# Kernel tuning notes

Measured on AMD Instinct MI355X. Metric: run time of the kernel, lower is better.

## Reference

```python
import jax, jax.numpy as jnp
import numpy as np

EPS = 1e-5       # norm_eps
CHUNK = 64       # scan checkpoint chunk size

def _short_conv(x, w):
    # causal depthwise conv (kernel K) + SiLU; x:[B,T,C], w:[C,K]
    K = w.shape[1]
    T = x.shape[1]
    xp = jnp.pad(x, ((0, 0), (K - 1, 0), (0, 0)))
    y = sum(xp[:, i:i + T, :] * w[:, i] for i in range(K))
    return jax.nn.silu(y)

def _l2norm(x):
    return x * jax.lax.rsqrt(jnp.sum(x * x, -1, keepdims=True) + 1e-6)

def _forward(hidden_states, Wq, Wk, Wv, conv_q, conv_k, conv_v, Wf1, Wf2, Wb,
             A_log, dt_bias, Wg, bg, o_norm_w, Wo):
    B, T, _ = hidden_states.shape
    H = A_log.shape[0]
    x = hidden_states
    q = _short_conv(x @ Wq, conv_q)
    k = _short_conv(x @ Wk, conv_k)
    v = _short_conv(x @ Wv, conv_v)
    Dk = q.shape[-1] // H
    Dv = v.shape[-1] // H
    q = _l2norm(q.reshape(B, T, H, Dk))
    k = _l2norm(k.reshape(B, T, H, Dk))
    v = v.reshape(B, T, H, Dv)
    beta = jax.nn.sigmoid(x @ Wb)                               # [B,T,H]
    g = ((x @ Wf1) @ Wf2).reshape(B, T, H, Dk)
    # KDA gate: g = -exp(A_log) * softplus(g + dt_bias), per head & key channel
    g = -jnp.exp(A_log)[:, None] * jax.nn.softplus(g + dt_bias.reshape(H, Dk))
    gexp = jnp.exp(g)                                           # decay in (0,1)
    scale = Dk ** -0.5

    def step(S, inp):
        q_t, k_t, v_t, ge_t, b_t = inp                          # [B,H,Dk]..., [B,H]
        S = S * ge_t[..., None]                                 # per-key-channel decay
        kv = jnp.einsum('bhk,bhkv->bhv', k_t, S)                # current prediction
        upd = (v_t - kv) * b_t[..., None]                       # delta-rule update
        S = S + jnp.einsum('bhk,bhv->bhkv', k_t, upd)
        o_t = jnp.einsum('bhk,bhkv->bhv', q_t, S) * scale
        return S, o_t

    @jax.checkpoint
    def chunk_fn(S, chunk):
        return jax.lax.scan(step, S, chunk)

    def tm(a):  # [B,T,...] -> [T//CHUNK, CHUNK, B, ...]
        a = jnp.moveaxis(a, 1, 0)
        return a.reshape((T // CHUNK, CHUNK) + a.shape[1:])

    S0 = jnp.zeros((B, H, Dk, Dv), dtype=q.dtype)
    _, o = jax.lax.scan(chunk_fn, S0, (tm(q), tm(k), tm(v), tm(gexp), tm(beta)))
    o = jnp.moveaxis(o.reshape((T, B, H, Dv)), 0, 1)            # [B,T,H,Dv]

    gate_o = (x @ Wg + bg).reshape(B, T, H, Dv)
    on = o * jax.lax.rsqrt(jnp.mean(o * o, -1, keepdims=True) + EPS) * o_norm_w
    on = on * jax.nn.silu(gate_o)                               # gated RMSNorm
    return on.reshape(B, T, H * Dv) @ Wo


def setup_inputs() -> dict:
    key = jax.random.key(0)
    ks = jax.random.split(key, 16)
    B, T, D = 2, 2048, 2048
    H, Dk, Dv, K = 16, 128, 128, 4
    n = jax.random.normal
    return {
        'hidden_states': n(ks[0], (B, T, D), jnp.float32),
        'Wq': n(ks[1], (D, H * Dk), jnp.float32) * D ** -0.5,
        'Wk': n(ks[2], (D, H * Dk), jnp.float32) * D ** -0.5,
        'Wv': n(ks[3], (D, H * Dv), jnp.float32) * D ** -0.5,
        'conv_q': n(ks[4], (H * Dk, K), jnp.float32) * 0.5,
        'conv_k': n(ks[5], (H * Dk, K), jnp.float32) * 0.5,
        'conv_v': n(ks[6], (H * Dv, K), jnp.float32) * 0.5,
        'Wf1': n(ks[7], (D, Dv), jnp.float32) * D ** -0.5,
        'Wf2': n(ks[8], (Dv, H * Dk), jnp.float32) * Dv ** -0.5,
        'Wb': n(ks[9], (D, H), jnp.float32) * D ** -0.5,
        'A_log': jnp.log(jax.random.uniform(ks[10], (H,), jnp.float32, 1.0, 16.0)),
        'dt_bias': jnp.zeros((H * Dk,), jnp.float32),
        'Wg': n(ks[11], (D, H * Dv), jnp.float32) * D ** -0.5,
        'bg': jnp.zeros((H * Dv,), jnp.float32),
        'o_norm_w': jnp.ones((Dv,), jnp.float32),
        'Wo': n(ks[12], (H * Dv, D), jnp.float32) * (H * Dv) ** -0.5,
    }


def reference(hidden_states, Wq, Wk, Wv, conv_q, conv_k, conv_v, Wf1, Wf2, Wb,
              A_log, dt_bias, Wg, bg, o_norm_w, Wo):
    return _forward(hidden_states, Wq, Wk, Wv, conv_q, conv_k, conv_v, Wf1, Wf2,
                    Wb, A_log, dt_bias, Wg, bg, o_norm_w, Wo)
```

## Files before the change

### kernel.cpp

```cpp
#include <hip/hip_runtime.h>
#include <stdint.h>

#define BB 2
#define TT 2048
#define DD 2048
#define HH 16
#define HD 2048
#define MM 4096
#define SCH 16

typedef float f32x4 __attribute__((ext_vector_type(4)));
typedef __bf16 bf16x8 __attribute__((ext_vector_type(8)));
typedef unsigned short u16x4 __attribute__((ext_vector_type(4)));

__device__ __forceinline__ unsigned short f2b(float f) {
  unsigned int u = __float_as_uint(f);
  u += 0x7FFFu + ((u >> 16) & 1u);
  return (unsigned short)(u >> 16);
}

__device__ __forceinline__ void async_ld16(const void* g, void* l) {
  typedef __attribute__((address_space(3))) void as3_t;
  typedef const __attribute__((address_space(1))) void as1_t;
  __builtin_amdgcn_global_load_lds((as1_t*)(uintptr_t)g,
                                   (as3_t*)(unsigned int)(uintptr_t)l, 16, 0, 0);
}

template <int CTRL>
__device__ __forceinline__ float dpp_add(float x) {
  int y = __builtin_amdgcn_update_dpp(0, __float_as_int(x), CTRL, 0xF, 0xF, false);
  return x + __int_as_float(y);
}
__device__ __forceinline__ float reduce16(float x) {
  x = dpp_add<0xB1>(x);
  x = dpp_add<0x4E>(x);
  x = dpp_add<0x124>(x);
  x = dpp_add<0x128>(x);
  return x;
}

__global__ __launch_bounds__(256) void cast_f32_bf16(const float* __restrict__ in,
                                                     unsigned short* __restrict__ out,
                                                     int n4) {
  int i = blockIdx.x * 256 + threadIdx.x;
  if (i >= n4) return;
  f32x4 v = *(const f32x4*)(in + (size_t)i * 4);
  u16x4 r;
  #pragma unroll
  for (int j = 0; j < 4; j++) r[j] = f2b(v[j]);
  *(u16x4*)(out + (size_t)i * 4) = r;
}

__global__ __launch_bounds__(256) void transpose_cast(const float* __restrict__ in,
                                                      unsigned short* __restrict__ out,
                                                      int R, int C) {
  __shared__ float tile[32][33];
  int bx = blockIdx.x * 32, by = blockIdx.y * 32;
  int tx = threadIdx.x, ty = threadIdx.y;
  #pragma unroll
  for (int i = 0; i < 32; i += 8)
    tile[ty + i][tx] = in[(size_t)(by + ty + i) * C + bx + tx];
  __syncthreads();
  #pragma unroll
  for (int i = 0; i < 32; i += 8)
    out[(size_t)(bx + ty + i) * R + by + tx] = f2b(tile[tx][ty + i]);
}

__global__ __launch_bounds__(256) void gemm_bf16(const unsigned short* __restrict__ A,
                                                 const unsigned short* __restrict__ Bt,
                                                 float* __restrict__ C,
                                                 const float* __restrict__ bias,
                                                 int M, int N, int K) {
  __shared__ __align__(16) unsigned short As[128 * 32];
  __shared__ __align__(16) unsigned short Bs[128 * 32];
  int tid = threadIdx.x;
  int l = tid & 63, w = tid >> 6;
  int row0 = blockIdx.y * 128, col0 = blockIdx.x * 128;
  int wm = (w >> 1) * 64, wn = (w & 1) * 64;
  const f32x4 fz = {0.f, 0.f, 0.f, 0.f};
  f32x4 acc[4][4];
  #pragma unroll
  for (int i = 0; i < 4; i++)
    #pragma unroll
    for (int j = 0; j < 4; j++) acc[i][j] = fz;

  int srow = l >> 2, skoff = (l & 3) * 8;
  int quad = l >> 4, mrow = l & 15;

  for (int kt = 0; kt < K; kt += 32) {
    #pragma unroll
    for (int i = 0; i < 2; i++) {
      int c = w * 2 + i;
      const unsigned short* gA = A + (size_t)(row0 + c * 16 + srow) * K + kt + skoff;
      const unsigned short* gB = Bt + (size_t)(col0 + c * 16 + srow) * K + kt + skoff;
      async_ld16(gA, As + c * 512);
      async_ld16(gB, Bs + c * 512);
    }
    __syncthreads();
    bf16x8 af[4], bfr[4];
    #pragma unroll
    for (int i = 0; i < 4; i++)
      af[i] = *(const bf16x8*)(As + (wm + i * 16 + mrow) * 32 + quad * 8);
    #pragma unroll
    for (int j = 0; j < 4; j++)
      bfr[j] = *(const bf16x8*)(Bs + (wn + j * 16 + mrow) * 32 + quad * 8);
    #pragma unroll
    for (int i = 0; i < 4; i++)
      #pragma unroll
      for (int j = 0; j < 4; j++)
        acc[i][j] = __builtin_amdgcn_mfma_f32_16x16x32_bf16(af[i], bfr[j], acc[i][j], 0, 0, 0);
    __syncthreads();
  }
  #pragma unroll
  for (int i = 0; i < 4; i++) {
    #pragma unroll
    for (int j = 0; j < 4; j++) {
      #pragma unroll
      for (int r = 0; r < 4; r++) {
        int rr = row0 + wm + i * 16 + quad * 4 + r;
        int cc = col0 + wn + j * 16 + mrow;
        float v = acc[i][j][r];
        if (bias) v += bias[cc];
        C[(size_t)rr * N + cc] = v;
      }
    }
  }
}

__global__ __launch_bounds__(256) void conv_silu_kernel(const float* __restrict__ Pre,
                                                        const float* __restrict__ cw,
                                                        float* __restrict__ outp,
                                                        int do_norm) {
  int bt = blockIdx.x;
  int b = bt >> 11, t = bt & (TT - 1);
  int tid = threadIdx.x;
  int ch0 = tid * 8;
  f32x4 wv[8];
  #pragma unroll
  for (int j = 0; j < 8; j++) wv[j] = *(const f32x4*)(cw + (size_t)(ch0 + j) * 4);
  float acc[8] = {0, 0, 0, 0, 0, 0, 0, 0};
  #pragma unroll
  for (int i = 0; i < 4; i++) {
    int tt = t - 3 + i;
    if (tt < 0) continue;
    const float* r = Pre + ((size_t)(b * TT + tt)) * HD + ch0;
    f32x4 a0 = *(const f32x4*)r;
    f32x4 a1 = *(const f32x4*)(r + 4);
    #pragma unroll
    for (int j = 0; j < 4; j++) {
      acc[j]     += a0[j] * wv[j][i];
      acc[4 + j] += a1[j] * wv[4 + j][i];
    }
  }
  float val[8];
  #pragma unroll
  for (int j = 0; j < 8; j++) val[j] = acc[j] / (1.f + expf(-acc[j]));
  if (do_norm) {
    float ss = 0.f;
    #pragma unroll
    for (int j = 0; j < 8; j++) ss += val[j] * val[j];
    ss = reduce16(ss);
    float rs = rsqrtf(ss + 1e-6f);
    #pragma unroll
    for (int j = 0; j < 8; j++) val[j] *= rs;
  }
  int h = tid >> 4, cc = (tid & 15) * 8;
  float* op = outp + (((size_t)(b * HH + h)) * TT + t) * 128 + cc;
  f32x4 o0, o1;
  #pragma unroll
  for (int j = 0; j < 4; j++) { o0[j] = val[j]; o1[j] = val[4 + j]; }
  *(f32x4*)op = o0;
  *(f32x4*)(op + 4) = o1;
}

__global__ __launch_bounds__(256) void beta_kernel(const float* __restrict__ x,
                                                   const float* __restrict__ Wb,
                                                   float* __restrict__ beta) {
  __shared__ float xs[2048];
  int bt = blockIdx.x, tid = threadIdx.x;
  int b = bt >> 11, t = bt & (TT - 1);
  const float* row = x + (size_t)bt * DD;
  #pragma unroll
  for (int i = 0; i < 2; i++)
    *(f32x4*)(xs + tid * 8 + i * 4) = *(const f32x4*)(row + tid * 8 + i * 4);
  __syncthreads();
  int h = tid >> 4, seg = tid & 15;
  float p = 0.f;
  for (int j = 0; j < 128; j++) {
    int d = seg * 128 + ((j + seg * 9) & 127);
    p += xs[d] * Wb[(size_t)d * HH + h];
  }
  p = reduce16(p);
  if (seg == 0) beta[((size_t)(b * HH + h)) * TT + t] = 1.f / (1.f + expf(-p));
}

__global__ __launch_bounds__(256) void gexp_kernel(const float* __restrict__ g,
                                                   const float* __restrict__ A_log,
                                                   const float* __restrict__ dt_bias,
                                                   float* __restrict__ ge, int n) {
  int i = blockIdx.x * 256 + threadIdx.x;
  if (i >= n) return;
  int bt = i >> 11, ch = i & (HD - 1);
  int b = bt >> 11, t = bt & (TT - 1);
  int h = ch >> 7, c = ch & 127;
  float gv = g[i] + dt_bias[ch];
  float sp = (gv > 20.f) ? gv : log1pf(expf(gv));
  ge[(((size_t)(b * HH + h)) * TT + t) * 128 + c] = expf(-expf(A_log[h]) * sp);
}

__global__ __launch_bounds__(256) void scan_kernel(const float* __restrict__ q,
                                                   const float* __restrict__ k,
                                                   const float* v,
                                                   const float* __restrict__ ge,
                                                   const float* __restrict__ beta,
                                                   float* o) {
  __shared__ __align__(16) float kbuf[2][SCH * 128];
  __shared__ __align__(16) float gbuf[2][SCH * 128];
  __shared__ __align__(16) float qbuf[2][SCH * 128];
  __shared__ __align__(16) float vbuf[2][SCH * 16];
  __shared__ __align__(16) float bbuf[TT];

  int blk = blockIdx.x;
  int colblk = blk & 7;
  int bh = blk >> 3;
  int tid = threadIdx.x;
  int w = tid >> 6, l = tid & 63;
  int grp = l >> 4, i = l & 15;
  int lcol = w * 4 + grp;
  int col = colblk * 16 + lcol;

  const float* kbh = k    + (size_t)bh * TT * 128;
  const float* gbh = ge   + (size_t)bh * TT * 128;
  const float* qbh = q    + (size_t)bh * TT * 128;
  const float* vbh = v    + (size_t)bh * TT * 128;
  const float* bbh = beta + (size_t)bh * TT;
  float* obh = o + (size_t)bh * TT * 128;

  #pragma unroll
  for (int j = 0; j < 2; j++) {
    int jj = w * 2 + j;
    async_ld16(bbh + jj * 256 + l * 4, (float*)bbuf + jj * 256);
  }
  if (w == 0) {
    #pragma unroll
    for (int j = 0; j < 8; j++)
      async_ld16(kbh + j * 256 + l * 4, (float*)kbuf[0] + j * 256);
  } else if (w == 1) {
    #pragma unroll
    for (int j = 0; j < 8; j++)
      async_ld16(gbh + j * 256 + l * 4, (float*)gbuf[0] + j * 256);
  } else if (w == 2) {
    #pragma unroll
    for (int j = 0; j < 8; j++)
      async_ld16(qbh + j * 256 + l * 4, (float*)qbuf[0] + j * 256);
  } else {
    async_ld16(vbh + (size_t)(l >> 2) * 128 + colblk * 16 + (l & 3) * 4,
               (float*)vbuf[0]);
  }
  __syncthreads();

  f32x4 s0 = {0.f, 0.f, 0.f, 0.f}, s1 = {0.f, 0.f, 0.f, 0.f};
  const float scale = 0.08838834764831845f;

  for (int c = 0; c < TT / SCH; c++) {
    int cb = c & 1, nb = cb ^ 1;
    if (c + 1 < TT / SCH) {
      size_t t0n = (size_t)(c + 1) * SCH;
      if (w == 0) {
        #pragma unroll
        for (int j = 0; j < 8; j++)
          async_ld16(kbh + t0n * 128 + j * 256 + l * 4, (float*)kbuf[nb] + j * 256);
      } else if (w == 1) {
        #pragma unroll
        for (int j = 0; j < 8; j++)
          async_ld16(gbh + t0n * 128 + j * 256 + l * 4, (float*)gbuf[nb] + j * 256);
      } else if (w == 2) {
        #pragma unroll
        for (int j = 0; j < 8; j++)
          async_ld16(qbh + t0n * 128 + j * 256 + l * 4, (float*)qbuf[nb] + j * 256);
      } else {
        async_ld16(vbh + (t0n + (l >> 2)) * 128 + colblk * 16 + (l & 3) * 4,
                   (float*)vbuf[nb]);
      }
    }
    const float* kc = (const float*)kbuf[cb];
    const float* gc = (const float*)gbuf[cb];
    const float* qc = (const float*)qbuf[cb];
    f32x4 k0 = *(const f32x4*)(kc + i * 8), k1 = *(const f32x4*)(kc + i * 8 + 4);
    f32x4 g0 = *(const f32x4*)(gc + i * 8), g1 = *(const f32x4*)(gc + i * 8 + 4);
    f32x4 q0 = *(const f32x4*)(qc + i * 8), q1 = *(const f32x4*)(qc + i * 8 + 4);
    #pragma unroll
    for (int s = 0; s < SCH; s++) {
      f32x4 k0n, k1n, g0n, g1n, q0n, q1n;
      if (s + 1 < SCH) {
        const float* kp = kc + (s + 1) * 128 + i * 8;
        const float* gp = gc + (s + 1) * 128 + i * 8;
        const float* qp = qc + (s + 1) * 128 + i * 8;
        k0n = *(const f32x4*)kp; k1n = *(const f32x4*)(kp + 4);
        g0n = *(const f32x4*)gp; g1n = *(const f32x4*)(gp + 4);
        q0n = *(const f32x4*)qp; q1n = *(const f32x4*)(qp + 4);
      }
      float vt = ((const float*)vbuf[cb])[s * 16 + lcol];
      float bt = ((const float*)bbuf)[c * SCH + s];
      s0 *= g0; s1 *= g1;
      f32x4 pp = k0 * s0 + k1 * s1;
      float p = (pp[0] + pp[1]) + (pp[2] + pp[3]);
      p = reduce16(p);
      float u = (vt - p) * bt;
      s0 += k0 * u; s1 += k1 * u;
      f32x4 oo = q0 * s0 + q1 * s1;
      float po = (oo[0] + oo[1]) + (oo[2] + oo[3]);
      po = reduce16(po);
      if (i == 0) obh[((size_t)c * SCH + s) * 128 + col] = po * scale;
      if (s + 1 < SCH) {
        k0 = k0n; k1 = k1n; g0 = g0n; g1 = g1n; q0 = q0n; q1 = q1n;
      }
    }
    __syncthreads();
  }
}

__global__ __launch_bounds__(256) void out_norm_kernel(const float* o,
                                                       const float* __restrict__ gate,
                                                       const float* __restrict__ w,
                                                       unsigned short* __restrict__ onb) {
  int bt = blockIdx.x, tid = threadIdx.x;
  int b = bt >> 11, t = bt & (TT - 1);
  int h = tid >> 4, seg = tid & 15;
  size_t obase = (((size_t)(b * HH + h)) * TT + t) * 128 + seg * 8;
  size_t gbase = (size_t)bt * HD + (size_t)h * 128 + seg * 8;
  f32x4 o0 = *(const f32x4*)(o + obase);
  f32x4 o1 = *(const f32x4*)(o + obase + 4);
  float ss = 0.f;
  #pragma unroll
  for (int j = 0; j < 4; j++) ss += o0[j] * o0[j] + o1[j] * o1[j];
  ss = reduce16(ss);
  float rs = rsqrtf(ss * (1.f / 128.f) + 1e-5f);
  u16x4 r0, r1;
  #pragma unroll
  for (int j = 0; j < 4; j++) {
    float gv0 = gate[gbase + j];
    float gv1 = gate[gbase + 4 + j];
    float a0 = o0[j] * rs * w[seg * 8 + j] * (gv0 / (1.f + expf(-gv0)));
    float a1 = o1[j] * rs * w[seg * 8 + 4 + j] * (gv1 / (1.f + expf(-gv1)));
    r0[j] = f2b(a0);
    r1[j] = f2b(a1);
  }
  *(u16x4*)(onb + gbase) = r0;
  *(u16x4*)(onb + gbase + 4) = r1;
}

extern "C" void kernel_launch(void* const* d_in, const int* in_sizes, int n_in,
                              void* d_out, int out_size, void* d_ws, size_t ws_size,
                              hipStream_t stream) {
  const float* x       = (const float*)d_in[0];
  const float* Wq      = (const float*)d_in[1];
  const float* Wk      = (const float*)d_in[2];
  const float* Wv      = (const float*)d_in[3];
  const float* cq      = (const float*)d_in[4];
  const float* ck      = (const float*)d_in[5];
  const float* cv      = (const float*)d_in[6];
  const float* Wf1     = (const float*)d_in[7];
  const float* Wf2     = (const float*)d_in[8];
  const float* Wb      = (const float*)d_in[9];
  const float* A_log   = (const float*)d_in[10];
  const float* dt_bias = (const float*)d_in[11];
  const float* Wg      = (const float*)d_in[12];
  const float* bg      = (const float*)d_in[13];
  const float* onw     = (const float*)d_in[14];
  const float* Wo      = (const float*)d_in[15];
  float* out = (float*)d_out;

  char* ws = (char*)d_ws;
  unsigned short* WT  = (unsigned short*)(ws);
  unsigned short* xb  = (unsigned short*)(ws + ((size_t)8  << 20));
  float* P    = (float*)(ws + ((size_t)24  << 20));
  float* qb   = (float*)(ws + ((size_t)56  << 20));
  float* kb   = (float*)(ws + ((size_t)88  << 20));
  float* vb   = (float*)(ws + ((size_t)120 << 20));
  float* geb  = (float*)(ws + ((size_t)152 << 20));
  float* betab= (float*)(ws + ((size_t)184 << 20));
  float* f1   = (float*)(ws + ((size_t)185 << 20));
  unsigned short* f1b = (unsigned short*)(ws + ((size_t)187 << 20));
  unsigned short* onb = xb;
  float* gateb = P;
  float* ob    = vb;

  dim3 tb(32, 8);
  dim3 gemm_grid(HD / 128, MM / 128);

  cast_f32_bf16<<<(MM * DD / 4 + 255) / 256, 256, 0, stream>>>(x, xb, MM * DD / 4);

  transpose_cast<<<dim3(HD / 32, DD / 32), tb, 0, stream>>>(Wq, WT, DD, HD);
  gemm_bf16<<<gemm_grid, 256, 0, stream>>>(xb, WT, P, nullptr, MM, HD, DD);
  conv_silu_kernel<<<MM, 256, 0, stream>>>(P, cq, qb, 1);
  transpose_cast<<<dim3(HD / 32, DD / 32), tb, 0, stream>>>(Wk, WT, DD, HD);
  gemm_bf16<<<gemm_grid, 256, 0, stream>>>(xb, WT, P, nullptr, MM, HD, DD);
  conv_silu_kernel<<<MM, 256, 0, stream>>>(P, ck, kb, 1);
  transpose_cast<<<dim3(HD / 32, DD / 32), tb, 0, stream>>>(Wv, WT, DD, HD);
  gemm_bf16<<<gemm_grid, 256, 0, stream>>>(xb, WT, P, nullptr, MM, HD, DD);
  conv_silu_kernel<<<MM, 256, 0, stream>>>(P, cv, vb, 0);

  beta_kernel<<<MM, 256, 0, stream>>>(x, Wb, betab);

  transpose_cast<<<dim3(128 / 32, DD / 32), tb, 0, stream>>>(Wf1, WT, DD, 128);
  gemm_bf16<<<dim3(1, MM / 128), 256, 0, stream>>>(xb, WT, f1, nullptr, MM, 128, DD);
  cast_f32_bf16<<<(MM * 128 / 4 + 255) / 256, 256, 0, stream>>>(f1, f1b, MM * 128 / 4);
  transpose_cast<<<dim3(HD / 32, 128 / 32), tb, 0, stream>>>(Wf2, WT, 128, HD);
  gemm_bf16<<<gemm_grid, 256, 0, stream>>>(f1b, WT, P, nullptr, MM, HD, 128);
  gexp_kernel<<<(MM * HD + 255) / 256, 256, 0, stream>>>(P, A_log, dt_bias, geb, MM * HD);

  transpose_cast<<<dim3(HD / 32, DD / 32), tb, 0, stream>>>(Wg, WT, DD, HD);
  gemm_bf16<<<gemm_grid, 256, 0, stream>>>(xb, WT, gateb, bg, MM, HD, DD);

  scan_kernel<<<BB * HH * 8, 256, 0, stream>>>(qb, kb, vb, geb, betab, ob);

  out_norm_kernel<<<MM, 256, 0, stream>>>(ob, gateb, onw, onb);

  transpose_cast<<<dim3(DD / 32, HD / 32), tb, 0, stream>>>(Wo, WT, HD, DD);
  gemm_bf16<<<dim3(DD / 128, MM / 128), 256, 0, stream>>>(onb, WT, out, nullptr, MM, DD, HD);
}
```

Baseline: 1.238 ms.

## Split scan state across 32 lanes per column with permlane32 reduction

The delta-rule scan kernel now spreads each value column's 128-entry state over 32 lanes (4 floats each) instead of 16 lanes (8 floats each). Blocks go to 512 threads with the same grid, which halves the serial per-lane work and the register state. Cross-lane dot products gain a permlane32_swap step after the DPP reduction. The block index mapping is also changed so neighbouring blocks hold different batch-heads, staging loads are spread across more waves, and the k·(g∘S) prediction is reordered. The risks are a longer reduction chain per step and the larger block cost from __syncthreads.

```diff
diff --git a/kernel.cpp b/kernel.cpp
--- a/kernel.cpp
+++ b/kernel.cpp
@@ -12,6 +12,7 @@
 typedef float f32x4 __attribute__((ext_vector_type(4)));
 typedef __bf16 bf16x8 __attribute__((ext_vector_type(8)));
 typedef unsigned short u16x4 __attribute__((ext_vector_type(4)));
+typedef unsigned int u32x2 __attribute__((ext_vector_type(2)));
 
 __device__ __forceinline__ unsigned short f2b(float f) {
   unsigned int u = __float_as_uint(f);
@@ -37,6 +38,12 @@
   x = dpp_add<0x124>(x);
   x = dpp_add<0x128>(x);
   return x;
+}
+
+__device__ __forceinline__ float swap32_sum(float x) {
+  u32x2 r = __builtin_amdgcn_permlane32_swap(__float_as_uint(x),
+                                             __float_as_uint(x), false, false);
+  return __uint_as_float(r.x) + __uint_as_float(r.y);
 }
 
 __global__ __launch_bounds__(256) void cast_f32_bf16(const float* __restrict__ in,
@@ -208,7 +215,7 @@
   ge[(((size_t)(b * HH + h)) * TT + t) * 128 + c] = expf(-expf(A_log[h]) * sp);
 }
 
-__global__ __launch_bounds__(256) void scan_kernel(const float* __restrict__ q,
+__global__ __launch_bounds__(512) void scan_kernel(const float* __restrict__ q,
                                                    const float* __restrict__ k,
                                                    const float* v,
                                                    const float* __restrict__ ge,
@@ -221,12 +228,13 @@
   __shared__ __align__(16) float bbuf[TT];
 
   int blk = blockIdx.x;
-  int colblk = blk & 7;
-  int bh = blk >> 3;
+  int bh = blk & 31;
+  int colblk = blk >> 5;
   int tid = threadIdx.x;
   int w = tid >> 6, l = tid & 63;
-  int grp = l >> 4, i = l & 15;
-  int lcol = w * 4 + grp;
+  int half = (l >> 4) & 1;
+  int i = (l & 15) | ((l & 32) >> 1);
+  int lcol = w * 2 + half;
   int col = colblk * 16 + lcol;
 
   const float* kbh = k    + (size_t)bh * TT * 128;
@@ -236,85 +244,77 @@
   const float* bbh = beta + (size_t)bh * TT;
   float* obh = o + (size_t)bh * TT * 128;
 
-  #pragma unroll
-  for (int j = 0; j < 2; j++) {
-    int jj = w * 2 + j;
-    async_ld16(bbh + jj * 256 + l * 4, (float*)bbuf + jj * 256);
-  }
-  if (w == 0) {
+  auto stage = [&](int cidx, int nb) {
+    size_t t0 = (size_t)cidx * SCH;
+    if (w < 2) {
+      int j0 = w * 4;
+      #pragma unroll
+      for (int j = 0; j < 4; j++)
+        async_ld16(kbh + t0 * 128 + (j0 + j) * 256 + l * 4,
+                   (float*)kbuf[nb] + (j0 + j) * 256);
+    } else if (w < 4) {
+      int j0 = (w - 2) * 4;
+      #pragma unroll
+      for (int j = 0; j < 4; j++)
+        async_ld16(gbh + t0 * 128 + (j0 + j) * 256 + l * 4,
+                   (float*)gbuf[nb] + (j0 + j) * 256);
+    } else if (w < 6) {
+      int j0 = (w - 4) * 4;
+      #pragma unroll
+      for (int j = 0; j < 4; j++)
+        async_ld16(qbh + t0 * 128 + (j0 + j) * 256 + l * 4,
+                   (float*)qbuf[nb] + (j0 + j) * 256);
+    } else if (w == 6) {
+      async_ld16(vbh + (t0 + (size_t)(l >> 2)) * 128 + colblk * 16 + (l & 3) * 4,
+                 (float*)vbuf[nb]);
+    }
+  };
+
+  if (w == 7) {
     #pragma unroll
     for (int j = 0; j < 8; j++)
-      async_ld16(kbh + j * 256 + l * 4, (float*)kbuf[0] + j * 256);
-  } else if (w == 1) {
-    #pragma unroll
-    for (int j = 0; j < 8; j++)
-      async_ld16(gbh + j * 256 + l * 4, (float*)gbuf[0] + j * 256);
-  } else if (w == 2) {
-    #pragma unroll
-    for (int j = 0; j < 8; j++)
-      async_ld16(qbh + j * 256 + l * 4, (float*)qbuf[0] + j * 256);
-  } else {
-    async_ld16(vbh + (size_t)(l >> 2) * 128 + colblk * 16 + (l & 3) * 4,
-               (float*)vbuf[0]);
-  }
+      async_ld16(bbh + j * 256 + l * 4, (float*)bbuf + j * 256);
+  }
+  stage(0, 0);
   __syncthreads();
 
-  f32x4 s0 = {0.f, 0.f, 0.f, 0.f}, s1 = {0.f, 0.f, 0.f, 0.f};
+  f32x4 sv = {0.f, 0.f, 0.f, 0.f};
   const float scale = 0.08838834764831845f;
 
   for (int c = 0; c < TT / SCH; c++) {
     int cb = c & 1, nb = cb ^ 1;
-    if (c + 1 < TT / SCH) {
-      size_t t0n = (size_t)(c + 1) * SCH;
-      if (w == 0) {
-        #pragma unroll
-        for (int j = 0; j < 8; j++)
-          async_ld16(kbh + t0n * 128 + j * 256 + l * 4, (float*)kbuf[nb] + j * 256);
-      } else if (w == 1) {
-        #pragma unroll
-        for (int j = 0; j < 8; j++)
-          async_ld16(gbh + t0n * 128 + j * 256 + l * 4, (float*)gbuf[nb] + j * 256);
-      } else if (w == 2) {
-        #pragma unroll
-        for (int j = 0; j < 8; j++)
-          async_ld16(qbh + t0n * 128 + j * 256 + l * 4, (float*)qbuf[nb] + j * 256);
-      } else {
-        async_ld16(vbh + (t0n + (l >> 2)) * 128 + colblk * 16 + (l & 3) * 4,
-                   (float*)vbuf[nb]);
-      }
-    }
+    if (c + 1 < TT / SCH) stage(c + 1, nb);
+
     const float* kc = (const float*)kbuf[cb];
     const float* gc = (const float*)gbuf[cb];
     const float* qc = (const float*)qbuf[cb];
-    f32x4 k0 = *(const f32x4*)(kc + i * 8), k1 = *(const f32x4*)(kc + i * 8 + 4);
-    f32x4 g0 = *(const f32x4*)(gc + i * 8), g1 = *(const f32x4*)(gc + i * 8 + 4);
-    f32x4 q0 = *(const f32x4*)(qc + i * 8), q1 = *(const f32x4*)(qc + i * 8 + 4);
+    f32x4 k4 = *(const f32x4*)(kc + i * 4);
+    f32x4 g4 = *(const f32x4*)(gc + i * 4);
+    f32x4 q4 = *(const f32x4*)(qc + i * 4);
     #pragma unroll
     for (int s = 0; s < SCH; s++) {
-      f32x4 k0n, k1n, g0n, g1n, q0n, q1n;
+      f32x4 k4n, g4n, q4n;
       if (s + 1 < SCH) {
-        const float* kp = kc + (s + 1) * 128 + i * 8;
-        const float* gp = gc + (s + 1) * 128 + i * 8;
-        const float* qp = qc + (s + 1) * 128 + i * 8;
-        k0n = *(const f32x4*)kp; k1n = *(const f32x4*)(kp + 4);
-        g0n = *(const f32x4*)gp; g1n = *(const f32x4*)(gp + 4);
-        q0n = *(const f32x4*)qp; q1n = *(const f32x4*)(qp + 4);
+        k4n = *(const f32x4*)(kc + (s + 1) * 128 + i * 4);
+        g4n = *(const f32x4*)(gc + (s + 1) * 128 + i * 4);
+        q4n = *(const f32x4*)(qc + (s + 1) * 128 + i * 4);
       }
       float vt = ((const float*)vbuf[cb])[s * 16 + lcol];
-      float bt = ((const float*)bbuf)[c * SCH + s];
-      s0 *= g0; s1 *= g1;
-      f32x4 pp = k0 * s0 + k1 * s1;
+      float bt = bbuf[c * SCH + s];
+      f32x4 kg = k4 * g4;
+      f32x4 pp = kg * sv;
       float p = (pp[0] + pp[1]) + (pp[2] + pp[3]);
       p = reduce16(p);
-      float u = (vt - p) * bt;
-      s0 += k0 * u; s1 += k1 * u;
-      f32x4 oo = q0 * s0 + q1 * s1;
+      p = swap32_sum(p);
+      sv *= g4;
+      float u = fmaf(-bt, p, vt * bt);
+      sv += k4 * u;
+      f32x4 oo = q4 * sv;
       float po = (oo[0] + oo[1]) + (oo[2] + oo[3]);
       po = reduce16(po);
+      po = swap32_sum(po);
       if (i == 0) obh[((size_t)c * SCH + s) * 128 + col] = po * scale;
-      if (s + 1 < SCH) {
-        k0 = k0n; k1 = k1n; g0 = g0n; g1 = g1n; q0 = q0n; q1 = q1n;
-      }
+      if (s + 1 < SCH) { k4 = k4n; g4 = g4n; q4 = q4n; }
     }
     __syncthreads();
   }
@@ -413,7 +413,7 @@
   transpose_cast<<<dim3(HD / 32, DD / 32), tb, 0, stream>>>(Wg, WT, DD, HD);
   gemm_bf16<<<gemm_grid, 256, 0, stream>>>(xb, WT, gateb, bg, MM, HD, DD);
 
-  scan_kernel<<<BB * HH * 8, 256, 0, stream>>>(qb, kb, vb, geb, betab, ob);
+  scan_kernel<<<BB * HH * 8, 512, 0, stream>>>(qb, kb, vb, geb, betab, ob);
 
   out_norm_kernel<<<MM, 256, 0, stream>>>(ob, gateb, onw, onb);
 
```

Result: slower. 1.306 ms (+5.5%).

## Swizzle scan LDS layout, batch output stores, fold scale into q

Applied to the files above, without the earlier changes.

The scan kernel now stages k, g and q chunks into shared memory with an XOR-swizzled layout to reduce bank conflicts on the per-lane 8-float reads. It also collects each of the 16 per-step outputs into one lane and writes them with a single store per chunk instead of a store per step. The v*beta product and the scale factor are precomputed (scale folded into the q normalization), the kg product is computed off the decay critical path, and the block-to-head mapping is reordered so that neighbouring blocks handle different heads. These changes aim to cut LDS conflicts and store overhead in the latency-bound recurrence, at the cost of slightly different floating-point rounding.

```diff
diff --git a/kernel.cpp b/kernel.cpp
--- a/kernel.cpp
+++ b/kernel.cpp
@@ -130,7 +130,7 @@
 __global__ __launch_bounds__(256) void conv_silu_kernel(const float* __restrict__ Pre,
                                                         const float* __restrict__ cw,
                                                         float* __restrict__ outp,
-                                                        int do_norm) {
+                                                        int do_norm, float post_mul) {
   int bt = blockIdx.x;
   int b = bt >> 11, t = bt & (TT - 1);
   int tid = threadIdx.x;
@@ -160,7 +160,7 @@
     #pragma unroll
     for (int j = 0; j < 8; j++) ss += val[j] * val[j];
     ss = reduce16(ss);
-    float rs = rsqrtf(ss + 1e-6f);
+    float rs = rsqrtf(ss + 1e-6f) * post_mul;
     #pragma unroll
     for (int j = 0; j < 8; j++) val[j] *= rs;
   }
@@ -221,13 +221,20 @@
   __shared__ __align__(16) float bbuf[TT];
 
   int blk = blockIdx.x;
-  int colblk = blk & 7;
-  int bh = blk >> 3;
+  int bh = blk & 31;
+  int colblk = blk >> 5;
   int tid = threadIdx.x;
   int w = tid >> 6, l = tid & 63;
   int grp = l >> 4, i = l & 15;
   int lcol = w * 4 + grp;
   int col = colblk * 16 + lcol;
+
+  int u0 = 2 * i, u1 = 2 * i + 1;
+  int of0 = (u0 ^ (u0 >> 3)) * 4;
+  int of1 = (u1 ^ (u1 >> 3)) * 4;
+  int su = l & 31;
+  int ssw = (su ^ (su >> 3)) * 4;
+  int srow2 = l >> 5;
 
   const float* kbh = k    + (size_t)bh * TT * 128;
   const float* gbh = ge   + (size_t)bh * TT * 128;
@@ -241,81 +248,79 @@
     int jj = w * 2 + j;
     async_ld16(bbh + jj * 256 + l * 4, (float*)bbuf + jj * 256);
   }
-  if (w == 0) {
-    #pragma unroll
-    for (int j = 0; j < 8; j++)
-      async_ld16(kbh + j * 256 + l * 4, (float*)kbuf[0] + j * 256);
-  } else if (w == 1) {
-    #pragma unroll
-    for (int j = 0; j < 8; j++)
-      async_ld16(gbh + j * 256 + l * 4, (float*)gbuf[0] + j * 256);
-  } else if (w == 2) {
-    #pragma unroll
-    for (int j = 0; j < 8; j++)
-      async_ld16(qbh + j * 256 + l * 4, (float*)qbuf[0] + j * 256);
-  } else {
-    async_ld16(vbh + (size_t)(l >> 2) * 128 + colblk * 16 + (l & 3) * 4,
-               (float*)vbuf[0]);
-  }
+  auto stage = [&](int cidx, int nb) {
+    size_t t0 = (size_t)cidx * SCH;
+    if (w == 0) {
+      #pragma unroll
+      for (int j = 0; j < 8; j++)
+        async_ld16(kbh + (t0 + j * 2 + srow2) * 128 + ssw,
+                   (float*)kbuf[nb] + j * 256);
+    } else if (w == 1) {
+      #pragma unroll
+      for (int j = 0; j < 8; j++)
+        async_ld16(gbh + (t0 + j * 2 + srow2) * 128 + ssw,
+                   (float*)gbuf[nb] + j * 256);
+    } else if (w == 2) {
+      #pragma unroll
+      for (int j = 0; j < 8; j++)
+        async_ld16(qbh + (t0 + j * 2 + srow2) * 128 + ssw,
+                   (float*)qbuf[nb] + j * 256);
+    } else {
+      async_ld16(vbh + (t0 + (size_t)(l >> 2)) * 128 + colblk * 16 + (l & 3) * 4,
+                 (float*)vbuf[nb]);
+    }
+  };
+  stage(0, 0);
   __syncthreads();
 
   f32x4 s0 = {0.f, 0.f, 0.f, 0.f}, s1 = {0.f, 0.f, 0.f, 0.f};
-  const float scale = 0.08838834764831845f;
+  float okeep = 0.f;
 
   for (int c = 0; c < TT / SCH; c++) {
     int cb = c & 1, nb = cb ^ 1;
-    if (c + 1 < TT / SCH) {
-      size_t t0n = (size_t)(c + 1) * SCH;
-      if (w == 0) {
-        #pragma unroll
-        for (int j = 0; j < 8; j++)
-          async_ld16(kbh + t0n * 128 + j * 256 + l * 4, (float*)kbuf[nb] + j * 256);
-      } else if (w == 1) {
-        #pragma unroll
-        for (int j = 0; j < 8; j++)
-          async_ld16(gbh + t0n * 128 + j * 256 + l * 4, (float*)gbuf[nb] + j * 256);
-      } else if (w == 2) {
-        #pragma unroll
-        for (int j = 0; j < 8; j++)
-          async_ld16(qbh + t0n * 128 + j * 256 + l * 4, (float*)qbuf[nb] + j * 256);
-      } else {
-        async_ld16(vbh + (t0n + (l >> 2)) * 128 + colblk * 16 + (l & 3) * 4,
-                   (float*)vbuf[nb]);
-      }
-    }
+    if (c + 1 < TT / SCH) stage(c + 1, nb);
+
     const float* kc = (const float*)kbuf[cb];
     const float* gc = (const float*)gbuf[cb];
     const float* qc = (const float*)qbuf[cb];
-    f32x4 k0 = *(const f32x4*)(kc + i * 8), k1 = *(const f32x4*)(kc + i * 8 + 4);
-    f32x4 g0 = *(const f32x4*)(gc + i * 8), g1 = *(const f32x4*)(gc + i * 8 + 4);
-    f32x4 q0 = *(const f32x4*)(qc + i * 8), q1 = *(const f32x4*)(qc + i * 8 + 4);
+    float vbt[SCH], btp[SCH];
+    #pragma unroll
+    for (int s = 0; s < SCH; s++) {
+      float vv = ((const float*)vbuf[cb])[s * 16 + lcol];
+      float bb = bbuf[c * SCH + s];
+      btp[s] = bb;
+      vbt[s] = vv * bb;
+    }
+    f32x4 k0 = *(const f32x4*)(kc + of0), k1 = *(const f32x4*)(kc + of1);
+    f32x4 g0 = *(const f32x4*)(gc + of0), g1 = *(const f32x4*)(gc + of1);
+    f32x4 q0 = *(const f32x4*)(qc + of0), q1 = *(const f32x4*)(qc + of1);
     #pragma unroll
     for (int s = 0; s < SCH; s++) {
       f32x4 k0n, k1n, g0n, g1n, q0n, q1n;
       if (s + 1 < SCH) {
-        const float* kp = kc + (s + 1) * 128 + i * 8;
-        const float* gp = gc + (s + 1) * 128 + i * 8;
-        const float* qp = qc + (s + 1) * 128 + i * 8;
-        k0n = *(const f32x4*)kp; k1n = *(const f32x4*)(kp + 4);
-        g0n = *(const f32x4*)gp; g1n = *(const f32x4*)(gp + 4);
-        q0n = *(const f32x4*)qp; q1n = *(const f32x4*)(qp + 4);
+        const float* kp = kc + (s + 1) * 128;
+        const float* gp = gc + (s + 1) * 128;
+        const float* qp = qc + (s + 1) * 128;
+        k0n = *(const f32x4*)(kp + of0); k1n = *(const f32x4*)(kp + of1);
+        g0n = *(const f32x4*)(gp + of0); g1n = *(const f32x4*)(gp + of1);
+        q0n = *(const f32x4*)(qp + of0); q1n = *(const f32x4*)(qp + of1);
       }
-      float vt = ((const float*)vbuf[cb])[s * 16 + lcol];
-      float bt = ((const float*)bbuf)[c * SCH + s];
-      s0 *= g0; s1 *= g1;
-      f32x4 pp = k0 * s0 + k1 * s1;
+      f32x4 kg0 = k0 * g0, kg1 = k1 * g1;
+      f32x4 pp = kg0 * s0 + kg1 * s1;
       float p = (pp[0] + pp[1]) + (pp[2] + pp[3]);
       p = reduce16(p);
-      float u = (vt - p) * bt;
+      s0 *= g0; s1 *= g1;
+      float u = fmaf(-btp[s], p, vbt[s]);
       s0 += k0 * u; s1 += k1 * u;
       f32x4 oo = q0 * s0 + q1 * s1;
       float po = (oo[0] + oo[1]) + (oo[2] + oo[3]);
       po = reduce16(po);
-      if (i == 0) obh[((size_t)c * SCH + s) * 128 + col] = po * scale;
+      okeep = (i == s) ? po : okeep;
       if (s + 1 < SCH) {
         k0 = k0n; k1 = k1n; g0 = g0n; g1 = g1n; q0 = q0n; q1 = q1n;
       }
     }
+    obh[((size_t)c * SCH + i) * 128 + col] = okeep;
     __syncthreads();
   }
 }
@@ -393,13 +398,13 @@
 
   transpose_cast<<<dim3(HD / 32, DD / 32), tb, 0, stream>>>(Wq, WT, DD, HD);
   gemm_bf16<<<gemm_grid, 256, 0, stream>>>(xb, WT, P, nullptr, MM, HD, DD);
-  conv_silu_kernel<<<MM, 256, 0, stream>>>(P, cq, qb, 1);
+  conv_silu_kernel<<<MM, 256, 0, stream>>>(P, cq, qb, 1, 0.08838834764831845f);
   transpose_cast<<<dim3(HD / 32, DD / 32), tb, 0, stream>>>(Wk, WT, DD, HD);
   gemm_bf16<<<gemm_grid, 256, 0, stream>>>(xb, WT, P, nullptr, MM, HD, DD);
-  conv_silu_kernel<<<MM, 256, 0, stream>>>(P, ck, kb, 1);
+  conv_silu_kernel<<<MM, 256, 0, stream>>>(P, ck, kb, 1, 1.0f);
   transpose_cast<<<dim3(HD / 32, DD / 32), tb, 0, stream>>>(Wv, WT, DD, HD);
   gemm_bf16<<<gemm_grid, 256, 0, stream>>>(xb, WT, P, nullptr, MM, HD, DD);
-  conv_silu_kernel<<<MM, 256, 0, stream>>>(P, cv, vb, 0);
+  conv_silu_kernel<<<MM, 256, 0, stream>>>(P, cv, vb, 0, 1.0f);
 
   beta_kernel<<<MM, 256, 0, stream>>>(x, Wb, betab);
 
```

After: 1.239 ms. No clear change (+0.1%).
